# Optimization experiments

Measured on AMD Instinct MI355X. Metric: run time of the kernel, lower is better.

Reference implementation:

```python
import jax, jax.numpy as jnp
import numpy as np

N, D, H, C, OUT = 50000, 128, 2, 128, 2   # nodes, in-feat, heads, per-head width, classes
E = 800000
HC = H * C
NEG_SLOPE = 0.2


def setup_inputs() -> dict:
    key = jax.random.key(0)
    ks = jax.random.split(key, 12)
    x = jax.random.normal(ks[0], (N, D), dtype=jnp.float32)
    edge_index = jax.random.randint(ks[1], (2, E), 0, N, dtype=jnp.int64)
    def w(k, fan_in, shape):
        return jax.random.normal(k, shape, dtype=jnp.float32) / np.sqrt(fan_in)
    return {
        "x": x,
        "edge_index": edge_index,
        # layer 0: in D -> H*C
        "W0": w(ks[2], D, (D, HC)),
        "att_src0": w(ks[3], C, (H, C)),
        "att_dst0": w(ks[4], C, (H, C)),
        "b0": jnp.zeros((HC,), dtype=jnp.float32),
        # layer 1: in H*C -> H*C
        "W1": w(ks[5], HC, (HC, HC)),
        "att_src1": w(ks[6], C, (H, C)),
        "att_dst1": w(ks[7], C, (H, C)),
        "b1": jnp.zeros((HC,), dtype=jnp.float32),
        # final linear: H*C -> OUT (concat GAT output)
        "Wl": w(ks[8], HC, (HC, OUT)),
        "bl": jnp.zeros((OUT,), dtype=jnp.float32),
    }


def _gat_layer(x, src, dst, W, att_src, att_dst, b):
    """PyG GATConv (concat=True, negative_slope=0.2, self-loops already in src/dst)."""
    n = x.shape[0]
    h = (x @ W).reshape(n, H, C)                       # [N,H,C]
    a_s = jnp.einsum("nhc,hc->nh", h, att_src)         # [N,H]
    a_d = jnp.einsum("nhc,hc->nh", h, att_dst)         # [N,H]
    logits = jax.nn.leaky_relu(a_s[src] + a_d[dst], NEG_SLOPE)  # [E',H]
    m = jax.ops.segment_max(logits, dst, num_segments=n)
    e = jnp.exp(logits - m[dst])
    denom = jax.ops.segment_sum(e, dst, num_segments=n)
    alpha = e / (denom[dst] + 1e-16)                   # softmax over incoming edges
    msg = h[src] * alpha[:, :, None]                   # [E',H,C]
    out = jax.ops.segment_sum(msg, dst, num_segments=n)
    return out.reshape(n, HC) + b


def reference(x, edge_index, W0, att_src0, att_dst0, b0,
              W1, att_src1, att_dst1, b1, Wl, bl):
    n = x.shape[0]
    loop = jnp.arange(n, dtype=edge_index.dtype)
    src = jnp.concatenate([edge_index[0], loop])       # add self loops (GATConv default)
    dst = jnp.concatenate([edge_index[1], loop])
    h = _gat_layer(x, src, dst, W0, att_src0, att_dst0, b0)
    h = jnp.tanh(h)                                    # tanh between layers only
    h = _gat_layer(h, src, dst, W1, att_src1, att_dst1, b1)
    out = h @ Wl + bl
    return jax.nn.softmax(out, axis=1)
```

## Files before the change

### kernel.cpp

```cpp
#include <hip/hip_runtime.h>
#include <math.h>

constexpr int N_NODES = 50000;
constexpr int N_EDGES = 800000;
constexpr int TOT_E   = N_EDGES + N_NODES;
constexpr int MAXD    = 256;

constexpr int GY      = (N_NODES + 63) / 64;
constexpr int GT_BLKS = GY * 4;

constexpr int PADSH = 5;

constexpr int PREP_CVT  = (N_NODES * 128 / 4 + 255) / 256;
constexpr int PREP_WT0  = 128;
constexpr int PREP_DEG  = (TOT_E + 255) / 256;
constexpr int PREP_SKIN = (N_NODES + 15) / 16;
constexpr int PREP_C    = 1;
constexpr int PREP_BLKS = PREP_CVT + PREP_WT0 + PREP_DEG + PREP_SKIN + PREP_C;

typedef __attribute__((ext_vector_type(8))) short bf16x8;
typedef __attribute__((ext_vector_type(4))) float f32x4;
typedef __attribute__((ext_vector_type(2))) float f32x2;

__device__ __forceinline__ unsigned short f2bf(float f) {
    unsigned int u = __float_as_uint(f);
    unsigned int r = (u + 0x7fffu + ((u >> 16) & 1u)) >> 16;
    return (unsigned short)r;
}
__device__ __forceinline__ unsigned int f2bf_pack(float lo, float hi) {
    return (unsigned int)f2bf(lo) | ((unsigned int)f2bf(hi) << 16);
}
__device__ __forceinline__ float bf2f_lo(unsigned int packed) {
    return __uint_as_float(packed << 16);
}
__device__ __forceinline__ float bf2f_hi(unsigned int packed) {
    return __uint_as_float(packed & 0xffff0000u);
}

__device__ __forceinline__ float lrelu(float x) { return x > 0.f ? x : 0.2f * x; }


__global__ __launch_bounds__(256) void zero_pre_k(uint4* __restrict__ degp4,
        int* __restrict__ total, float* __restrict__ c2,
        const float* __restrict__ W0, const float* __restrict__ att_src0,
        const float* __restrict__ att_dst0,
        const float* __restrict__ W1, const float* __restrict__ att_src1,
        const float* __restrict__ att_dst1, const float* __restrict__ Wl,
        float* __restrict__ w0buf, float* __restrict__ pv) {
    int i = blockIdx.x * blockDim.x + threadIdx.x;
    if (i < N_NODES * 32 / 4) degp4[i] = make_uint4(0, 0, 0, 0);
    if (blockIdx.x == 0) {
        if (threadIdx.x == 0) { *total = 0; c2[0] = 0.f; c2[1] = 0.f; }
        int k = threadIdx.x;
        float v0 = 0, v1 = 0, v2 = 0, v3 = 0, v4 = 0, v5 = 0, v6 = 0, v7 = 0;
        const float* wr = W1 + (size_t)k * 256;
        for (int c = 0; c < 128; ++c) {
            float wv = wr[c];
            v0 = fmaf(wv, att_src1[c], v0);
            v2 = fmaf(wv, att_dst1[c], v2);
            v4 = fmaf(wv, Wl[c * 2 + 0], v4);
            v5 = fmaf(wv, Wl[c * 2 + 1], v5);
        }
        for (int c = 128; c < 256; ++c) {
            float wv = wr[c];
            v1 = fmaf(wv, att_src1[c], v1);
            v3 = fmaf(wv, att_dst1[c], v3);
            v6 = fmaf(wv, Wl[c * 2 + 0], v6);
            v7 = fmaf(wv, Wl[c * 2 + 1], v7);
        }
        float* p = pv + (size_t)k * 8;
        p[0] = v0; p[1] = v1; p[2] = v2; p[3] = v3;
        p[4] = v4; p[5] = v5; p[6] = v6; p[7] = v7;
        if (k < 128) {
            float w0v = 0, w1v = 0, w2v = 0, w3v = 0;
            const float* wr0 = W0 + (size_t)k * 256;
            for (int c = 0; c < 128; ++c) {
                float wv = wr0[c];
                w0v = fmaf(wv, att_src0[c], w0v);
                w2v = fmaf(wv, att_dst0[c], w2v);
            }
            for (int c = 128; c < 256; ++c) {
                float wv = wr0[c];
                w1v = fmaf(wv, att_src0[c], w1v);
                w3v = fmaf(wv, att_dst0[c], w3v);
            }
            float* q = w0buf + (size_t)k * 4;
            q[0] = w0v; q[1] = w1v; q[2] = w2v; q[3] = w3v;
        }
    }
}


__global__ __launch_bounds__(256) void prep_k(const float* __restrict__ x,
        unsigned short* __restrict__ xb, const float* __restrict__ W0,
        unsigned short* __restrict__ WT0, const int* __restrict__ ei,
        int* __restrict__ degp,
        const float* __restrict__ w0buf, float* __restrict__ a_s,
        float* __restrict__ a_d, const float* __restrict__ Wl,
        const float* __restrict__ b1, const float* __restrict__ bl,
        float* __restrict__ c2) {
    int b = blockIdx.x;
    if (b < PREP_CVT) {
        int i = b * 256 + threadIdx.x;
        if (i < N_NODES * 128 / 4) {
            float4 v = *reinterpret_cast<const float4*>(x + (size_t)i * 4);
            ushort4 o;
            o.x = f2bf(v.x); o.y = f2bf(v.y); o.z = f2bf(v.z); o.w = f2bf(v.w);
            *reinterpret_cast<ushort4*>(xb + (size_t)i * 4) = o;
        }
        return;
    }
    b -= PREP_CVT;
    if (b < PREP_WT0) {
        int idx = b * 256 + threadIdx.x;
        int k = idx >> 8, n = idx & 255;
        WT0[(size_t)n * 128 + k] = f2bf(W0[idx]);
        return;
    }
    b -= PREP_WT0;
    if (b < PREP_DEG) {
        int e = b * 256 + threadIdx.x;
        if (e < TOT_E) {
            int dst = (e < N_EDGES) ? ei[N_EDGES + e] : (e - N_EDGES);
            atomicAdd(&degp[dst << PADSH], 1);
        }
        return;
    }
    b -= PREP_DEG;
    if (b < PREP_SKIN) {
        int lane = threadIdx.x & 63;
        int sub = lane >> 4;
        int lq = lane & 15;
        int node = b * 16 + (threadIdx.x >> 6) * 4 + sub;
        if (node < N_NODES) {
            const float* xr = x + (size_t)node * 128 + lq * 8;
            const float4* wv = reinterpret_cast<const float4*>(w0buf) + lq * 8;
            float s0 = 0, s1 = 0, d0 = 0, d1 = 0;
#pragma unroll
            for (int t = 0; t < 8; ++t) {
                float xv = xr[t];
                float4 w = wv[t];
                s0 = fmaf(xv, w.x, s0);
                s1 = fmaf(xv, w.y, s1);
                d0 = fmaf(xv, w.z, d0);
                d1 = fmaf(xv, w.w, d1);
            }
#pragma unroll
            for (int off = 1; off < 16; off <<= 1) {
                s0 += __shfl_xor(s0, off);
                s1 += __shfl_xor(s1, off);
                d0 += __shfl_xor(d0, off);
                d1 += __shfl_xor(d1, off);
            }
            if (lq == 0) {
                *reinterpret_cast<float2*>(a_s + node * 2) = make_float2(s0, s1);
                *reinterpret_cast<float2*>(a_d + node * 2) = make_float2(d0, d1);
            }
        }
        return;
    }
    {
        int k = threadIdx.x;
        int lane = k & 63;
        float bv = b1[k];
        float p0 = bv * Wl[k * 2 + 0];
        float p1 = bv * Wl[k * 2 + 1];
        if (k == 0) { p0 += bl[0]; p1 += bl[1]; }
#pragma unroll
        for (int off = 32; off; off >>= 1) {
            p0 += __shfl_xor(p0, off);
            p1 += __shfl_xor(p1, off);
        }
        if (lane == 0) {
            atomicAdd(&c2[0], p0);
            atomicAdd(&c2[1], p1);
        }
    }
}


__global__ void offsets_k(const int* __restrict__ degp, int* __restrict__ start,
                          int* __restrict__ deg, int* __restrict__ cursorp,
                          int* __restrict__ total) {
    int lane = threadIdx.x & 63;
    int node = blockIdx.x * blockDim.x + threadIdx.x;
    int d = (node < N_NODES) ? degp[node << PADSH] : 0;
    int pre = d;
#pragma unroll
    for (int off = 1; off < 64; off <<= 1) {
        int v = __shfl_up(pre, off);
        if (lane >= off) pre += v;
    }
    int wtot = __shfl(pre, 63);
    int base = 0;
    if (lane == 63) base = atomicAdd(total, wtot);
    base = __shfl(base, 63);
    int my = base + pre - d;
    if (node < N_NODES) {
        start[node] = my;
        deg[node] = d;
        cursorp[node << PADSH] = my;
    }
}

__global__ __launch_bounds__(256) void scatter_k(const int* __restrict__ ei,
                                                 int* __restrict__ cursorp,
                                                 int* __restrict__ colv) {
    const int t = blockIdx.x * 256 + threadIdx.x;
    const int e0 = t * 4;
    if (e0 >= TOT_E) return;
    int srcs[4], dsts[4];
    if (e0 + 3 < N_EDGES) {
        int4 sv = *reinterpret_cast<const int4*>(ei + e0);
        int4 dv = *reinterpret_cast<const int4*>(ei + N_EDGES + e0);
        srcs[0] = sv.x; srcs[1] = sv.y; srcs[2] = sv.z; srcs[3] = sv.w;
        dsts[0] = dv.x; dsts[1] = dv.y; dsts[2] = dv.z; dsts[3] = dv.w;
#pragma unroll
        for (int k = 0; k < 4; ++k) {
            int pos = atomicAdd(&cursorp[dsts[k] << PADSH], 1);
            colv[pos] = srcs[k];
        }
    } else {
#pragma unroll
        for (int k = 0; k < 4; ++k) {
            int e = e0 + k;
            if (e < TOT_E) {
                int srcv, dstv;
                if (e < N_EDGES) { srcv = ei[e]; dstv = ei[N_EDGES + e]; }
                else             { srcv = dstv = e - N_EDGES; }
                int pos = atomicAdd(&cursorp[dstv << PADSH], 1);
                colv[pos] = srcv;
            }
        }
    }
}


__global__ __launch_bounds__(256) void agg0x_k(const unsigned short* __restrict__ xb,
                      const float* __restrict__ a_s, const float* __restrict__ a_d,
                      const int* __restrict__ start, const int* __restrict__ deg,
                      const int* __restrict__ colv,
                      unsigned short* __restrict__ xagg) {
    __shared__ float lexp[4][MAXD][2];
    const int lane = threadIdx.x & 63;
    const int wslot = threadIdx.x >> 6;
    const int node = blockIdx.x * 4 + wslot;
    if (node >= N_NODES) return;
    const int beg = start[node];
    const int degv = deg[node];
    const float ad0 = a_d[node * 2], ad1 = a_d[node * 2 + 1];
    const int* __restrict__ col = colv + beg;

    if (degv <= MAXD) {
        float s0 = 0.f, s1 = 0.f;
        for (int j = lane; j < degv; j += 64) {
            int s = col[j];
            float2 av = *reinterpret_cast<const float2*>(a_s + s * 2);
            float e0 = __expf(lrelu(av.x + ad0));
            float e1 = __expf(lrelu(av.y + ad1));
            *reinterpret_cast<float2*>(&lexp[wslot][j][0]) = make_float2(e0, e1);
            s0 += e0;
            s1 += e1;
        }
#pragma unroll
        for (int off = 32; off; off >>= 1) {
            s0 += __shfl_xor(s0, off);
            s1 += __shfl_xor(s1, off);
        }
        const float inv0 = 1.f / (s0 + 1e-16f);
        const float inv1 = 1.f / (s1 + 1e-16f);

        const int q = lane >> 4;
        const int lq = lane & 15;
        const unsigned short* __restrict__ xp = xb + lq * 8;
        f32x2 aA[4] = {};
        f32x2 aB[4] = {};
        const int full = degv >> 2;
        for (int i = 0; i < full; ++i) {
            const int j = 4 * i + q;
            const int s = col[j];
            float2 ee = *reinterpret_cast<float2*>(&lexp[wslot][j][0]);
            const uint4 hv = *reinterpret_cast<const uint4*>(xp + (size_t)s * 128);
            const f32x2 al0 = {ee.x, ee.x};
            const f32x2 al1 = {ee.y, ee.y};
            f32x2 p;
            p.x = bf2f_lo(hv.x); p.y = bf2f_hi(hv.x);
            aA[0] = __builtin_elementwise_fma(p, al0, aA[0]);
            aB[0] = __builtin_elementwise_fma(p, al1, aB[0]);
            p.x = bf2f_lo(hv.y); p.y = bf2f_hi(hv.y);
            aA[1] = __builtin_elementwise_fma(p, al0, aA[1]);
            aB[1] = __builtin_elementwise_fma(p, al1, aB[1]);
            p.x = bf2f_lo(hv.z); p.y = bf2f_hi(hv.z);
            aA[2] = __builtin_elementwise_fma(p, al0, aA[2]);
            aB[2] = __builtin_elementwise_fma(p, al1, aB[2]);
            p.x = bf2f_lo(hv.w); p.y = bf2f_hi(hv.w);
            aA[3] = __builtin_elementwise_fma(p, al0, aA[3]);
            aB[3] = __builtin_elementwise_fma(p, al1, aB[3]);
        }
        {
            const int j = full * 4 + q;
            if (j < degv) {
                const int s = col[j];
                float2 ee = *reinterpret_cast<float2*>(&lexp[wslot][j][0]);
                const uint4 hv = *reinterpret_cast<const uint4*>(xp + (size_t)s * 128);
                const f32x2 al0 = {ee.x, ee.x};
                const f32x2 al1 = {ee.y, ee.y};
                f32x2 p;
                p.x = bf2f_lo(hv.x); p.y = bf2f_hi(hv.x);
                aA[0] = __builtin_elementwise_fma(p, al0, aA[0]);
                aB[0] = __builtin_elementwise_fma(p, al1, aB[0]);
                p.x = bf2f_lo(hv.y); p.y = bf2f_hi(hv.y);
                aA[1] = __builtin_elementwise_fma(p, al0, aA[1]);
                aB[1] = __builtin_elementwise_fma(p, al1, aB[1]);
                p.x = bf2f_lo(hv.z); p.y = bf2f_hi(hv.z);
                aA[2] = __builtin_elementwise_fma(p, al0, aA[2]);
                aB[2] = __builtin_elementwise_fma(p, al1, aB[2]);
                p.x = bf2f_lo(hv.w); p.y = bf2f_hi(hv.w);
                aA[3] = __builtin_elementwise_fma(p, al0, aA[3]);
                aB[3] = __builtin_elementwise_fma(p, al1, aB[3]);
            }
        }
        float acc[16];
#pragma unroll
        for (int c = 0; c < 4; ++c) {
            acc[2 * c]     = aA[c].x;
            acc[2 * c + 1] = aA[c].y;
            acc[8 + 2 * c]     = aB[c].x;
            acc[8 + 2 * c + 1] = aB[c].y;
        }
#pragma unroll
        for (int c = 0; c < 16; ++c) {
            acc[c] += __shfl_xor(acc[c], 16);
            acc[c] += __shfl_xor(acc[c], 32);
        }
        if (lane < 16) {
#pragma unroll
            for (int c = 0; c < 8; ++c)  acc[c] *= inv0;
#pragma unroll
            for (int c = 8; c < 16; ++c) acc[c] *= inv1;
            uint4 v0, v1;
            v0.x = f2bf_pack(acc[0], acc[1]);
            v0.y = f2bf_pack(acc[2], acc[3]);
            v0.z = f2bf_pack(acc[4], acc[5]);
            v0.w = f2bf_pack(acc[6], acc[7]);
            v1.x = f2bf_pack(acc[8], acc[9]);
            v1.y = f2bf_pack(acc[10], acc[11]);
            v1.z = f2bf_pack(acc[12], acc[13]);
            v1.w = f2bf_pack(acc[14], acc[15]);
            *reinterpret_cast<uint4*>(xagg + (size_t)node * 256 + lq * 8) = v0;
            *reinterpret_cast<uint4*>(xagg + (size_t)node * 256 + 128 + lq * 8) = v1;
        }
    } else {
        const int end = beg + degv;
        float m0 = -INFINITY, m1 = -INFINITY;
        for (int e = beg + lane; e < end; e += 64) {
            int s = colv[e];
            m0 = fmaxf(m0, lrelu(a_s[s * 2] + ad0));
            m1 = fmaxf(m1, lrelu(a_s[s * 2 + 1] + ad1));
        }
#pragma unroll
        for (int off = 32; off; off >>= 1) {
            m0 = fmaxf(m0, __shfl_xor(m0, off));
            m1 = fmaxf(m1, __shfl_xor(m1, off));
        }
        float s0 = 0.f, s1 = 0.f;
        for (int e = beg + lane; e < end; e += 64) {
            int s = colv[e];
            s0 += __expf(lrelu(a_s[s * 2] + ad0) - m0);
            s1 += __expf(lrelu(a_s[s * 2 + 1] + ad1) - m1);
        }
#pragma unroll
        for (int off = 32; off; off >>= 1) {
            s0 += __shfl_xor(s0, off);
            s1 += __shfl_xor(s1, off);
        }
        float inv0 = 1.f / (s0 + 1e-16f);
        float inv1 = 1.f / (s1 + 1e-16f);
        const int cbase = lane * 2;
        float a00 = 0.f, a01 = 0.f, a10 = 0.f, a11 = 0.f;
        for (int e = beg; e < end; ++e) {
            int s = colv[e];
            float2 av = *reinterpret_cast<const float2*>(a_s + s * 2);
            float al0 = __expf(lrelu(av.x + ad0) - m0) * inv0;
            float al1 = __expf(lrelu(av.y + ad1) - m1) * inv1;
            unsigned int xv = *reinterpret_cast<const unsigned int*>(
                xb + (size_t)s * 128 + cbase);
            float x0 = bf2f_lo(xv), x1 = bf2f_hi(xv);
            a00 = fmaf(x0, al0, a00);
            a01 = fmaf(x1, al0, a01);
            a10 = fmaf(x0, al1, a10);
            a11 = fmaf(x1, al1, a11);
        }
        *reinterpret_cast<unsigned int*>(xagg + (size_t)node * 256 + cbase) =
            f2bf_pack(a00, a01);
        *reinterpret_cast<unsigned int*>(xagg + (size_t)node * 256 + 128 + cbase) =
            f2bf_pack(a10, a11);
    }
}


__global__ __launch_bounds__(256) void gemm_tanh_k(
        const unsigned short* __restrict__ A,
        const unsigned short* __restrict__ BT,
        const float* __restrict__ b0,
        const float* __restrict__ pv,
        float* __restrict__ part, int M) {
    const int bid = blockIdx.x;
    const int cb = bid & 3;
    const int gy = bid >> 2;
    const int head = cb >> 1;
    const int lane = threadIdx.x & 63;
    const int wv = threadIdx.x >> 6;
    const int lm = lane & 15;
    const int g8 = (lane >> 4) * 8;
    const int row0 = gy * 64 + wv * 16;
    const int n0 = cb * 64;

    int ra0 = row0 + lm;
    if (ra0 >= M) ra0 = M - 1;
    const unsigned short* pa0 = A + (size_t)ra0 * 256 + head * 128 + g8;
    const unsigned short* pb  = BT + (size_t)(n0 + lm) * 128 + g8;

    f32x4 acc[4] = {};
#pragma unroll
    for (int kt = 0; kt < 128; kt += 32) {
        bf16x8 a0 = *reinterpret_cast<const bf16x8*>(pa0 + kt);
        bf16x8 b0f = *reinterpret_cast<const bf16x8*>(pb + kt);
        bf16x8 b1f = *reinterpret_cast<const bf16x8*>(pb + 16 * 128 + kt);
        bf16x8 b2f = *reinterpret_cast<const bf16x8*>(pb + 32 * 128 + kt);
        bf16x8 b3f = *reinterpret_cast<const bf16x8*>(pb + 48 * 128 + kt);
        acc[0] = __builtin_amdgcn_mfma_f32_16x16x32_bf16(a0, b0f, acc[0], 0, 0, 0);
        acc[1] = __builtin_amdgcn_mfma_f32_16x16x32_bf16(a0, b1f, acc[1], 0, 0, 0);
        acc[2] = __builtin_amdgcn_mfma_f32_16x16x32_bf16(a0, b2f, acc[2], 0, 0, 0);
        acc[3] = __builtin_amdgcn_mfma_f32_16x16x32_bf16(a0, b3f, acc[3], 0, 0, 0);
    }

    float bc[4];
    float4 pA[4], pB[4];
#pragma unroll
    for (int j = 0; j < 4; ++j) {
        int c = n0 + j * 16 + lm;
        bc[j] = b0[c];
        pA[j] = *reinterpret_cast<const float4*>(pv + (size_t)c * 8);
        pB[j] = *reinterpret_cast<const float4*>(pv + (size_t)c * 8 + 4);
    }

    float pr[8][4];
#pragma unroll
    for (int p = 0; p < 8; ++p)
#pragma unroll
        for (int r = 0; r < 4; ++r) pr[p][r] = 0.f;
#pragma unroll
    for (int j = 0; j < 4; ++j)
#pragma unroll
        for (int r = 0; r < 4; ++r) {
            float th = tanhf(acc[j][r] + bc[j]);
            pr[0][r] = fmaf(th, pA[j].x, pr[0][r]);
            pr[1][r] = fmaf(th, pA[j].y, pr[1][r]);
            pr[2][r] = fmaf(th, pA[j].z, pr[2][r]);
            pr[3][r] = fmaf(th, pA[j].w, pr[3][r]);
            pr[4][r] = fmaf(th, pB[j].x, pr[4][r]);
            pr[5][r] = fmaf(th, pB[j].y, pr[5][r]);
            pr[6][r] = fmaf(th, pB[j].z, pr[6][r]);
            pr[7][r] = fmaf(th, pB[j].w, pr[7][r]);
        }
#pragma unroll
    for (int off = 1; off < 16; off <<= 1)
#pragma unroll
        for (int p = 0; p < 8; ++p)
#pragma unroll
            for (int r = 0; r < 4; ++r)
                pr[p][r] += __shfl_xor(pr[p][r], off);
    if (lm == 0) {
        int rb = row0 + (lane >> 4) * 4;
#pragma unroll
        for (int r = 0; r < 4; ++r) {
            if (rb + r < M) {
                float4* dst = reinterpret_cast<float4*>(
                    part + ((size_t)cb * N_NODES + rb + r) * 8);
                dst[0] = make_float4(pr[0][r], pr[1][r], pr[2][r], pr[3][r]);
                dst[1] = make_float4(pr[4][r], pr[5][r], pr[6][r], pr[7][r]);
            }
        }
    }
}


__global__ void reduce_part_k(const float* __restrict__ part,
                              float* __restrict__ asd1) {
    int i = blockIdx.x * blockDim.x + threadIdx.x;
    if (i < N_NODES * 8) {
        const size_t S = (size_t)N_NODES * 8;
        asd1[i] = part[i] + part[i + S] + part[i + 2 * S] + part[i + 3 * S];
    }
}


__global__ __launch_bounds__(256) void agg_final_k(
        const float* __restrict__ asd1, const int* __restrict__ start,
        const int* __restrict__ deg, const int* __restrict__ colv,
        const float* __restrict__ c2, float* __restrict__ out) {
    const int lane = threadIdx.x & 63;
    const int node = blockIdx.x * 4 + (threadIdx.x >> 6);
    if (node >= N_NODES) return;
    const int beg = start[node];
    const int degv = deg[node];
    const float ad0 = asd1[node * 8 + 2];
    const float ad1v = asd1[node * 8 + 3];
    const int* __restrict__ col = colv + beg;

    float s0 = 0.f, s1 = 0.f, A00 = 0.f, A01 = 0.f, A10 = 0.f, A11 = 0.f;
    for (int j = lane; j < degv; j += 64) {
        int s = col[j];
        const float* rs = asd1 + (size_t)s * 8;
        float2 av = *reinterpret_cast<const float2*>(rs);
        float4 gv = *reinterpret_cast<const float4*>(rs + 4);
        float e0 = __expf(lrelu(av.x + ad0));
        float e1 = __expf(lrelu(av.y + ad1v));
        s0 += e0;
        s1 += e1;
        A00 = fmaf(e0, gv.x, A00);
        A01 = fmaf(e0, gv.y, A01);
        A10 = fmaf(e1, gv.z, A10);
        A11 = fmaf(e1, gv.w, A11);
    }
#pragma unroll
    for (int off = 32; off; off >>= 1) {
        s0  += __shfl_xor(s0, off);
        s1  += __shfl_xor(s1, off);
        A00 += __shfl_xor(A00, off);
        A01 += __shfl_xor(A01, off);
        A10 += __shfl_xor(A10, off);
        A11 += __shfl_xor(A11, off);
    }
    if (lane == 0) {
        float i0 = 1.f / (s0 + 1e-16f), i1 = 1.f / (s1 + 1e-16f);
        float z0 = A00 * i0 + A10 * i1 + c2[0];
        float z1 = A01 * i0 + A11 * i1 + c2[1];
        float mx = fmaxf(z0, z1);
        float e0 = __expf(z0 - mx), e1 = __expf(z1 - mx);
        float inv = 1.f / (e0 + e1);
        out[node * 2 + 0] = e0 * inv;
        out[node * 2 + 1] = e1 * inv;
    }
}


extern "C" void kernel_launch(void* const* d_in, const int* in_sizes, int n_in,
                              void* d_out, int out_size, void* d_ws, size_t ws_size,
                              hipStream_t stream) {
    const float* x        = (const float*)d_in[0];
    const int*   ei       = (const int*)d_in[1];
    const float* W0       = (const float*)d_in[2];
    const float* att_src0 = (const float*)d_in[3];
    const float* att_dst0 = (const float*)d_in[4];
    const float* b0       = (const float*)d_in[5];
    const float* W1       = (const float*)d_in[6];
    const float* att_src1 = (const float*)d_in[7];
    const float* att_dst1 = (const float*)d_in[8];
    const float* b1       = (const float*)d_in[9];
    const float* Wl       = (const float*)d_in[10];
    const float* bl       = (const float*)d_in[11];
    float* out = (float*)d_out;

    unsigned short* xb   = (unsigned short*)d_ws;
    unsigned short* xagg = xb + (size_t)N_NODES * 128;
    unsigned short* WT0  = xagg + (size_t)N_NODES * 256;
    float* w0buf = (float*)(WT0 + 256 * 128);
    float* pv    = w0buf + 128 * 4;
    float* as0   = pv + 256 * 8;
    float* ad0   = as0 + N_NODES * 2;
    float* asd1  = ad0 + N_NODES * 2;
    float* part  = asd1 + (size_t)N_NODES * 8;
    int*   degp  = (int*)(part + (size_t)N_NODES * 32);
    int* cursorp = degp + (size_t)N_NODES * 32;
    int* deg     = cursorp + (size_t)N_NODES * 32;
    int* start   = deg + N_NODES;
    int* total   = start + N_NODES;
    float* c2    = (float*)(total + 1);
    int* colv    = (int*)(c2 + 2);

    zero_pre_k<<<(N_NODES * 32 / 4 + 255) / 256, 256, 0, stream>>>(
        (uint4*)degp, total, c2, W0, att_src0, att_dst0,
        W1, att_src1, att_dst1, Wl, w0buf, pv);

    prep_k<<<PREP_BLKS, 256, 0, stream>>>(x, xb, W0, WT0, ei, degp,
                                          w0buf, as0, ad0, Wl, b1, bl, c2);

    offsets_k<<<(N_NODES + 255) / 256, 256, 0, stream>>>(degp, start, deg, cursorp, total);
    scatter_k<<<(TOT_E + 1023) / 1024, 256, 0, stream>>>(ei, cursorp, colv);

    int nn4 = (N_NODES + 3) / 4;

    agg0x_k<<<nn4, 256, 0, stream>>>(xb, as0, ad0, start, deg, colv, xagg);
    gemm_tanh_k<<<GT_BLKS, 256, 0, stream>>>(xagg, WT0, b0, pv, part, N_NODES);
    reduce_part_k<<<(N_NODES * 8 + 255) / 256, 256, 0, stream>>>(part, asd1);

    agg_final_k<<<nn4, 256, 0, stream>>>(asd1, start, deg, colv, c2, out);
}
```

Before: 254.2 us.

## Split degree counting out and merge conversion prep work into scatter kernel

Degree counting is moved into its own small kernel that runs before the offsets scan. The independent preprocessing work (x to bf16 conversion, W0 transpose, attention score precompute, bias constant) is merged with the CSR scatter into one block-partitioned kernel. Prep and scatter then share a single launch, so the bandwidth-bound conversion can overlap the atomic-heavy scatter. In exchange the degree-count atomics lose their overlap with the conversion work, and the kernel count stays the same.

```diff
diff --git a/kernel.cpp b/kernel.cpp
--- a/kernel.cpp
+++ b/kernel.cpp
@@ -11,12 +11,12 @@
 
 constexpr int PADSH = 5;
 
-constexpr int PREP_CVT  = (N_NODES * 128 / 4 + 255) / 256;
-constexpr int PREP_WT0  = 128;
-constexpr int PREP_DEG  = (TOT_E + 255) / 256;
-constexpr int PREP_SKIN = (N_NODES + 15) / 16;
-constexpr int PREP_C    = 1;
-constexpr int PREP_BLKS = PREP_CVT + PREP_WT0 + PREP_DEG + PREP_SKIN + PREP_C;
+constexpr int MEGA_SC   = (TOT_E / 4 + 255) / 256 + 1;
+constexpr int MEGA_CVT  = (N_NODES * 128 / 4 + 255) / 256;
+constexpr int MEGA_WT0  = 128;
+constexpr int MEGA_SKIN = (N_NODES + 15) / 16;
+constexpr int MEGA_C    = 1;
+constexpr int MEGA_BLKS = MEGA_SC + MEGA_CVT + MEGA_WT0 + MEGA_SKIN + MEGA_C;
 
 typedef __attribute__((ext_vector_type(8))) short bf16x8;
 typedef __attribute__((ext_vector_type(4))) float f32x4;
@@ -91,91 +91,12 @@
 }
 
 
-__global__ __launch_bounds__(256) void prep_k(const float* __restrict__ x,
-        unsigned short* __restrict__ xb, const float* __restrict__ W0,
-        unsigned short* __restrict__ WT0, const int* __restrict__ ei,
-        int* __restrict__ degp,
-        const float* __restrict__ w0buf, float* __restrict__ a_s,
-        float* __restrict__ a_d, const float* __restrict__ Wl,
-        const float* __restrict__ b1, const float* __restrict__ bl,
-        float* __restrict__ c2) {
-    int b = blockIdx.x;
-    if (b < PREP_CVT) {
-        int i = b * 256 + threadIdx.x;
-        if (i < N_NODES * 128 / 4) {
-            float4 v = *reinterpret_cast<const float4*>(x + (size_t)i * 4);
-            ushort4 o;
-            o.x = f2bf(v.x); o.y = f2bf(v.y); o.z = f2bf(v.z); o.w = f2bf(v.w);
-            *reinterpret_cast<ushort4*>(xb + (size_t)i * 4) = o;
-        }
-        return;
-    }
-    b -= PREP_CVT;
-    if (b < PREP_WT0) {
-        int idx = b * 256 + threadIdx.x;
-        int k = idx >> 8, n = idx & 255;
-        WT0[(size_t)n * 128 + k] = f2bf(W0[idx]);
-        return;
-    }
-    b -= PREP_WT0;
-    if (b < PREP_DEG) {
-        int e = b * 256 + threadIdx.x;
-        if (e < TOT_E) {
-            int dst = (e < N_EDGES) ? ei[N_EDGES + e] : (e - N_EDGES);
-            atomicAdd(&degp[dst << PADSH], 1);
-        }
-        return;
-    }
-    b -= PREP_DEG;
-    if (b < PREP_SKIN) {
-        int lane = threadIdx.x & 63;
-        int sub = lane >> 4;
-        int lq = lane & 15;
-        int node = b * 16 + (threadIdx.x >> 6) * 4 + sub;
-        if (node < N_NODES) {
-            const float* xr = x + (size_t)node * 128 + lq * 8;
-            const float4* wv = reinterpret_cast<const float4*>(w0buf) + lq * 8;
-            float s0 = 0, s1 = 0, d0 = 0, d1 = 0;
-#pragma unroll
-            for (int t = 0; t < 8; ++t) {
-                float xv = xr[t];
-                float4 w = wv[t];
-                s0 = fmaf(xv, w.x, s0);
-                s1 = fmaf(xv, w.y, s1);
-                d0 = fmaf(xv, w.z, d0);
-                d1 = fmaf(xv, w.w, d1);
-            }
-#pragma unroll
-            for (int off = 1; off < 16; off <<= 1) {
-                s0 += __shfl_xor(s0, off);
-                s1 += __shfl_xor(s1, off);
-                d0 += __shfl_xor(d0, off);
-                d1 += __shfl_xor(d1, off);
-            }
-            if (lq == 0) {
-                *reinterpret_cast<float2*>(a_s + node * 2) = make_float2(s0, s1);
-                *reinterpret_cast<float2*>(a_d + node * 2) = make_float2(d0, d1);
-            }
-        }
-        return;
-    }
-    {
-        int k = threadIdx.x;
-        int lane = k & 63;
-        float bv = b1[k];
-        float p0 = bv * Wl[k * 2 + 0];
-        float p1 = bv * Wl[k * 2 + 1];
-        if (k == 0) { p0 += bl[0]; p1 += bl[1]; }
-#pragma unroll
-        for (int off = 32; off; off >>= 1) {
-            p0 += __shfl_xor(p0, off);
-            p1 += __shfl_xor(p1, off);
-        }
-        if (lane == 0) {
-            atomicAdd(&c2[0], p0);
-            atomicAdd(&c2[1], p1);
-        }
-    }
+__global__ __launch_bounds__(256) void degcnt_k(const int* __restrict__ ei,
+                                                int* __restrict__ degp) {
+    int e = blockIdx.x * blockDim.x + threadIdx.x;
+    if (e >= TOT_E) return;
+    int dst = (e < N_EDGES) ? ei[N_EDGES + e] : (e - N_EDGES);
+    atomicAdd(&degp[dst << PADSH], 1);
 }
 
 
@@ -203,34 +124,111 @@
     }
 }
 
-__global__ __launch_bounds__(256) void scatter_k(const int* __restrict__ ei,
-                                                 int* __restrict__ cursorp,
-                                                 int* __restrict__ colv) {
-    const int t = blockIdx.x * 256 + threadIdx.x;
-    const int e0 = t * 4;
-    if (e0 >= TOT_E) return;
-    int srcs[4], dsts[4];
-    if (e0 + 3 < N_EDGES) {
-        int4 sv = *reinterpret_cast<const int4*>(ei + e0);
-        int4 dv = *reinterpret_cast<const int4*>(ei + N_EDGES + e0);
-        srcs[0] = sv.x; srcs[1] = sv.y; srcs[2] = sv.z; srcs[3] = sv.w;
-        dsts[0] = dv.x; dsts[1] = dv.y; dsts[2] = dv.z; dsts[3] = dv.w;
-#pragma unroll
-        for (int k = 0; k < 4; ++k) {
-            int pos = atomicAdd(&cursorp[dsts[k] << PADSH], 1);
-            colv[pos] = srcs[k];
-        }
-    } else {
-#pragma unroll
-        for (int k = 0; k < 4; ++k) {
-            int e = e0 + k;
-            if (e < TOT_E) {
-                int srcv, dstv;
-                if (e < N_EDGES) { srcv = ei[e]; dstv = ei[N_EDGES + e]; }
-                else             { srcv = dstv = e - N_EDGES; }
-                int pos = atomicAdd(&cursorp[dstv << PADSH], 1);
-                colv[pos] = srcv;
-            }
+
+__global__ __launch_bounds__(256) void mega_k(const int* __restrict__ ei,
+        int* __restrict__ cursorp, int* __restrict__ colv,
+        const float* __restrict__ x, unsigned short* __restrict__ xb,
+        const float* __restrict__ W0, unsigned short* __restrict__ WT0,
+        const float* __restrict__ w0buf, float* __restrict__ a_s,
+        float* __restrict__ a_d, const float* __restrict__ Wl,
+        const float* __restrict__ b1, const float* __restrict__ bl,
+        float* __restrict__ c2) {
+    int b = blockIdx.x;
+    if (b < MEGA_SC) {
+        const int t = b * 256 + threadIdx.x;
+        const int e0 = t * 4;
+        if (e0 >= TOT_E) return;
+        if (e0 + 3 < N_EDGES) {
+            int4 sv = *reinterpret_cast<const int4*>(ei + e0);
+            int4 dv = *reinterpret_cast<const int4*>(ei + N_EDGES + e0);
+            int srcs[4] = {sv.x, sv.y, sv.z, sv.w};
+            int dsts[4] = {dv.x, dv.y, dv.z, dv.w};
+#pragma unroll
+            for (int k = 0; k < 4; ++k) {
+                int pos = atomicAdd(&cursorp[dsts[k] << PADSH], 1);
+                colv[pos] = srcs[k];
+            }
+        } else {
+#pragma unroll
+            for (int k = 0; k < 4; ++k) {
+                int e = e0 + k;
+                if (e < TOT_E) {
+                    int srcv, dstv;
+                    if (e < N_EDGES) { srcv = ei[e]; dstv = ei[N_EDGES + e]; }
+                    else             { srcv = dstv = e - N_EDGES; }
+                    int pos = atomicAdd(&cursorp[dstv << PADSH], 1);
+                    colv[pos] = srcv;
+                }
+            }
+        }
+        return;
+    }
+    b -= MEGA_SC;
+    if (b < MEGA_CVT) {
+        int i = b * 256 + threadIdx.x;
+        if (i < N_NODES * 128 / 4) {
+            float4 v = *reinterpret_cast<const float4*>(x + (size_t)i * 4);
+            ushort4 o;
+            o.x = f2bf(v.x); o.y = f2bf(v.y); o.z = f2bf(v.z); o.w = f2bf(v.w);
+            *reinterpret_cast<ushort4*>(xb + (size_t)i * 4) = o;
+        }
+        return;
+    }
+    b -= MEGA_CVT;
+    if (b < MEGA_WT0) {
+        int idx = b * 256 + threadIdx.x;
+        int k = idx >> 8, n = idx & 255;
+        WT0[(size_t)n * 128 + k] = f2bf(W0[idx]);
+        return;
+    }
+    b -= MEGA_WT0;
+    if (b < MEGA_SKIN) {
+        int lane = threadIdx.x & 63;
+        int sub = lane >> 4;
+        int lq = lane & 15;
+        int node = b * 16 + (threadIdx.x >> 6) * 4 + sub;
+        if (node < N_NODES) {
+            const float* xr = x + (size_t)node * 128 + lq * 8;
+            const float4* wv = reinterpret_cast<const float4*>(w0buf) + lq * 8;
+            float s0 = 0, s1 = 0, d0 = 0, d1 = 0;
+#pragma unroll
+            for (int t = 0; t < 8; ++t) {
+                float xv = xr[t];
+                float4 w = wv[t];
+                s0 = fmaf(xv, w.x, s0);
+                s1 = fmaf(xv, w.y, s1);
+                d0 = fmaf(xv, w.z, d0);
+                d1 = fmaf(xv, w.w, d1);
+            }
+#pragma unroll
+            for (int off = 1; off < 16; off <<= 1) {
+                s0 += __shfl_xor(s0, off);
+                s1 += __shfl_xor(s1, off);
+                d0 += __shfl_xor(d0, off);
+                d1 += __shfl_xor(d1, off);
+            }
+            if (lq == 0) {
+                *reinterpret_cast<float2*>(a_s + node * 2) = make_float2(s0, s1);
+                *reinterpret_cast<float2*>(a_d + node * 2) = make_float2(d0, d1);
+            }
+        }
+        return;
+    }
+    {
+        int k = threadIdx.x;
+        int lane = k & 63;
+        float bv = b1[k];
+        float p0 = bv * Wl[k * 2 + 0];
+        float p1 = bv * Wl[k * 2 + 1];
+        if (k == 0) { p0 += bl[0]; p1 += bl[1]; }
+#pragma unroll
+        for (int off = 32; off; off >>= 1) {
+            p0 += __shfl_xor(p0, off);
+            p1 += __shfl_xor(p1, off);
+        }
+        if (lane == 0) {
+            atomicAdd(&c2[0], p0);
+            atomicAdd(&c2[1], p1);
         }
     }
 }
@@ -584,11 +582,12 @@
         (uint4*)degp, total, c2, W0, att_src0, att_dst0,
         W1, att_src1, att_dst1, Wl, w0buf, pv);
 
-    prep_k<<<PREP_BLKS, 256, 0, stream>>>(x, xb, W0, WT0, ei, degp,
-                                          w0buf, as0, ad0, Wl, b1, bl, c2);
-
+    degcnt_k<<<(TOT_E + 255) / 256, 256, 0, stream>>>(ei, degp);
     offsets_k<<<(N_NODES + 255) / 256, 256, 0, stream>>>(degp, start, deg, cursorp, total);
-    scatter_k<<<(TOT_E + 1023) / 1024, 256, 0, stream>>>(ei, cursorp, colv);
+
+    mega_k<<<MEGA_BLKS, 256, 0, stream>>>(ei, cursorp, colv,
+                                          x, xb, W0, WT0, w0buf, as0, ad0,
+                                          Wl, b1, bl, c2);
 
     int nn4 = (N_NODES + 3) / 4;
 
```

Measured after the change: 260.9 us. 2.6% more time.
